# Kernel tuning notes

Hardware: AMD Instinct MI355X
Metric: run time of the kernel (lower is better)

## Reference

```python
import jax, jax.numpy as jnp
import numpy as np

N_NODES = 100000
N_EDGES = 1600000
IN_DIM = 128
HIDDEN = 128
OUT_DIM = 10
N_GRAPHS = 512
N_LAYERS = 3


def setup_inputs() -> dict:
    key = jax.random.key(0)
    ks = jax.random.split(key, 12)
    s_in = 1.0 / np.sqrt(IN_DIM)
    s_h = 1.0 / np.sqrt(HIDDEN)
    return {
        "x": jax.random.normal(ks[0], (N_NODES, IN_DIM), jnp.float32),
        "lin1_w": jax.random.normal(ks[1], (IN_DIM, HIDDEN), jnp.float32) * s_in,
        "lin1_b": jnp.zeros((HIDDEN,), jnp.float32),
        "gcn_w": jax.random.normal(ks[2], (N_LAYERS, HIDDEN, HIDDEN), jnp.float32) * s_h,
        "gcn_b": jnp.zeros((N_LAYERS, HIDDEN), jnp.float32),
        "lin_out_w": jax.random.normal(ks[3], (HIDDEN, HIDDEN), jnp.float32) * s_h,
        "lin_out_b": jnp.zeros((HIDDEN,), jnp.float32),
        "cls_w": jax.random.normal(ks[4], (HIDDEN, OUT_DIM), jnp.float32) * s_h,
        "cls_b": jnp.zeros((OUT_DIM,), jnp.float32),
        "edge_index": jax.random.randint(ks[5], (2, N_EDGES), 0, N_NODES, jnp.int64),
        "batch": jnp.sort(jax.random.randint(ks[6], (N_NODES,), 0, N_GRAPHS, jnp.int64)),
    }


def reference(x, lin1_w, lin1_b, gcn_w, gcn_b, lin_out_w, lin_out_b, cls_w, cls_b, edge_index, batch):
    n = x.shape[0]
    # GCNConv normalization with added self-loops (PyG default)
    row, col = edge_index[0], edge_index[1]
    loop = jnp.arange(n)
    row2 = jnp.concatenate([row, loop])  # source (message origin)
    col2 = jnp.concatenate([col, loop])  # target (aggregation index)
    deg = jax.ops.segment_sum(jnp.ones_like(col2, dtype=x.dtype), col2, num_segments=n)
    dinv = jax.lax.rsqrt(jnp.maximum(deg, 1.0))
    norm = (dinv[row2] * dinv[col2])[:, None]  # [E+N, 1]

    counts = jax.ops.segment_sum(jnp.ones((n,), x.dtype), batch, num_segments=N_GRAPHS)
    counts = jnp.maximum(counts, 1.0)[:, None]

    def readout_mean(h):  # global_mean_pool -> [G, H]
        return jax.ops.segment_sum(h, batch, num_segments=N_GRAPHS) / counts

    # lin1 + elu (dropout = identity in eval mode)
    h = jax.nn.elu(x @ lin1_w + lin1_b)
    reps = readout_mean(h)  # readout_layers[0]; l_sum accumulates layer reps
    for i in range(N_LAYERS):
        hw = h @ gcn_w[i]                       # [N, H]
        msg = norm * hw[row2]                   # gather + scale
        agg = jax.ops.segment_sum(msg, col2, num_segments=n)  # scatter-add
        h = jax.nn.elu(agg + gcn_b[i])          # GCNConv bias then NaOp act
        # pooling op is 'none' (remove_pooling=True): graph unchanged
        reps = reps + readout_mean(h)           # readout_layers[i+1], summed by LaOp 'l_sum'
    g = jax.nn.elu(reps @ lin_out_w + lin_out_b)
    logits = g @ cls_w + cls_b
    return jax.nn.log_softmax(logits, axis=-1)
```

## Files before the change

### kernel.cpp

```cpp
#include <hip/hip_runtime.h>
#include <hip/hip_bf16.h>
#include <math.h>

#define NN 100000
#define NE 1600000
#define HID 128
#define NG 512
#define NB 512
#define RB 196
#define PCHUNK 16384
#define NPARTB ((NE + PCHUNK - 1) / PCHUNK)
#define GEMM_GRID ((NN + 127) / 128)

typedef unsigned short ushort_t;
typedef __attribute__((ext_vector_type(8))) short bf16x8;
typedef __attribute__((ext_vector_type(8))) unsigned short ushort8_t;
typedef __attribute__((ext_vector_type(4))) float f32x4;

__device__ __forceinline__ ushort_t f2bf(float v) {
    unsigned u = __float_as_uint(v);
    unsigned r = (u + 0x7FFF + ((u >> 16) & 1)) >> 16;
    return (ushort_t)r;
}
__device__ __forceinline__ float bf2f(ushort_t u) {
    return __uint_as_float((unsigned)u << 16);
}


__global__ __launch_bounds__(256) void hist_prepw(const int* __restrict__ ecol, int* __restrict__ bcount,
                                                  const float* __restrict__ lin1_w,
                                                  const float* __restrict__ gcn_w,
                                                  ushort_t* __restrict__ wt_hi,
                                                  ushort_t* __restrict__ wt_lo) {
    if (blockIdx.x < NPARTB) {
        __shared__ int lh[NB];
        const int blk = blockIdx.x, t = threadIdx.x;
        for (int i = t; i < NB; i += 256) lh[i] = 0;
        __syncthreads();
        const int e0 = blk * PCHUNK;
        const int e1 = min(e0 + PCHUNK, NE);
        for (int e = e0 + t; e < e1; e += 256) atomicAdd(&lh[ecol[e] / RB], 1);
        __syncthreads();
        for (int i = t; i < NB; i += 256) bcount[blk * NB + i] = lh[i];
    } else {
        int mb = blockIdx.x - NPARTB;
        int m = mb >> 3;
        int chunk = mb & 7;
        const float* W = (m == 0) ? lin1_w : gcn_w + (size_t)(m - 1) * 16384;
        ushort_t* hi = wt_hi + (size_t)m * 16384;
        ushort_t* lo = wt_lo + (size_t)m * 16384;
        for (int i = chunk * 2048 + threadIdx.x; i < (chunk + 1) * 2048; i += 256) {
            int j = i & 7;
            int lane = (i >> 3) & 63;
            int ks = (i >> 9) & 3;
            int ct = (i >> 11) & 7;
            int n = ct * 16 + (lane & 15);
            int k = ks * 32 + (lane >> 4) * 8 + j;
            float v = W[k * 128 + n];
            ushort_t h = f2bf(v);
            hi[i] = h;
            lo[i] = f2bf(v - bf2f(h));
        }
    }
}

__global__ __launch_bounds__(NB) void scan_bases(const int* __restrict__ bcount, int* __restrict__ basew,
                                                 int* __restrict__ brp, int* __restrict__ rp,
                                                 const int* __restrict__ batch, float* __restrict__ invcnt) {
    __shared__ int s[NB];
    int t = threadIdx.x;
    int tot = 0;
    for (int k = 0; k < NPARTB; ++k) {
        int c = bcount[k * NB + t];
        basew[k * NB + t] = tot;
        tot += c;
    }
    s[t] = tot;
    __syncthreads();
    for (int off = 1; off < NB; off <<= 1) {
        int x = (t >= off) ? s[t - off] : 0;
        __syncthreads();
        s[t] += x;
        __syncthreads();
    }
    int ex = s[t] - tot;
    brp[t] = ex;
    if (t == NB - 1) { brp[NB] = s[t]; rp[NN] = s[t]; }

    int lo = 0, hi = NN;
    while (lo < hi) { int m = (lo + hi) >> 1; if (batch[m] < t) lo = m + 1; else hi = m; }
    int s0 = lo;
    lo = 0; hi = NN;
    while (lo < hi) { int m = (lo + hi) >> 1; if (batch[m] < t + 1) lo = m + 1; else hi = m; }
    int c = lo - s0;
    invcnt[t] = 1.0f / (float)(c > 0 ? c : 1);
}

template<bool F32A, int MODE>
__device__ __forceinline__ void gemm_body(int bid, int tid,
                                          const float* __restrict__ A,
                                          const ushort_t* __restrict__ a_bf,
                                          const ushort_t* __restrict__ wt_hi,
                                          const ushort_t* __restrict__ wt_lo,
                                          const float* __restrict__ bias,
                                          const float* __restrict__ dinv,
                                          ushort_t* __restrict__ out0,
                                          int N) {
    const int lane = tid & 63;
    const int wid = tid >> 6;
    const int rowBase = bid * 128 + wid * 32;
    const int rblk = rowBase >> 4;
    const int l15 = lane & 15, lg = lane >> 4;

    f32x4 acc[2][8];
#pragma unroll
    for (int rt = 0; rt < 2; ++rt)
#pragma unroll
        for (int ct = 0; ct < 8; ++ct) acc[rt][ct] = (f32x4){0.f, 0.f, 0.f, 0.f};

#pragma unroll
    for (int ks = 0; ks < 4; ++ks) {
        bf16x8 ahi[2], alo[2];
#pragma unroll
        for (int rt = 0; rt < 2; ++rt) {
            int r = rowBase + rt * 16 + l15;
            if (F32A) {
                float av[8];
                if (r < N) {
                    const float* ap = A + (size_t)r * 128 + ks * 32 + lg * 8;
                    float4 a0 = *(const float4*)(ap);
                    float4 a1 = *(const float4*)(ap + 4);
                    av[0] = a0.x; av[1] = a0.y; av[2] = a0.z; av[3] = a0.w;
                    av[4] = a1.x; av[5] = a1.y; av[6] = a1.z; av[7] = a1.w;
                } else {
#pragma unroll
                    for (int j = 0; j < 8; ++j) av[j] = 0.f;
                }
#pragma unroll
                for (int j = 0; j < 8; ++j) {
                    ushort_t h = f2bf(av[j]);
                    ahi[rt][j] = (short)h;
                    alo[rt][j] = (short)f2bf(av[j] - bf2f(h));
                }
            } else {
                if (r < N) {
                    ahi[rt] = *(const bf16x8*)(a_bf + (size_t)(rblk + rt) * 2048 + (ks * 4 + lg) * 128 + l15 * 8);
                } else {
                    bf16x8 z = {0, 0, 0, 0, 0, 0, 0, 0};
                    ahi[rt] = z;
                }
            }
        }
#pragma unroll
        for (int ct = 0; ct < 8; ++ct) {
            size_t boff = (size_t)(((ct * 4 + ks) * 64 + lane) * 8);
            bf16x8 bhi = *(const bf16x8*)(wt_hi + boff);
            bf16x8 blo = *(const bf16x8*)(wt_lo + boff);
            acc[0][ct] = __builtin_amdgcn_mfma_f32_16x16x32_bf16(ahi[0], bhi, acc[0][ct], 0, 0, 0);
            acc[1][ct] = __builtin_amdgcn_mfma_f32_16x16x32_bf16(ahi[1], bhi, acc[1][ct], 0, 0, 0);
            acc[0][ct] = __builtin_amdgcn_mfma_f32_16x16x32_bf16(ahi[0], blo, acc[0][ct], 0, 0, 0);
            acc[1][ct] = __builtin_amdgcn_mfma_f32_16x16x32_bf16(ahi[1], blo, acc[1][ct], 0, 0, 0);
            if (F32A) {
                acc[0][ct] = __builtin_amdgcn_mfma_f32_16x16x32_bf16(alo[0], bhi, acc[0][ct], 0, 0, 0);
                acc[1][ct] = __builtin_amdgcn_mfma_f32_16x16x32_bf16(alo[1], bhi, acc[1][ct], 0, 0, 0);
            }
        }
    }

#pragma unroll
    for (int rt = 0; rt < 2; ++rt) {
#pragma unroll
        for (int reg = 0; reg < 4; ++reg) {
            int row = rowBase + rt * 16 + lg * 4 + reg;
            if (row >= N) continue;
            if (MODE == 0) {
                int r16 = lg * 4 + reg;
#pragma unroll
                for (int ct = 0; ct < 8; ++ct) {
                    int colc = ct * 16 + l15;
                    float v = acc[rt][ct][reg] + bias[colc];
                    v = v > 0.f ? v : expf(v) - 1.f;
                    out0[(size_t)(rblk + rt) * 2048 + (colc >> 3) * 128 + r16 * 8 + (colc & 7)] = f2bf(v);
                }
            } else {
                float dv = dinv[row];
#pragma unroll
                for (int ct = 0; ct < 8; ++ct) {
                    int colc = ct * 16 + l15;
                    out0[(size_t)row * 128 + colc] = f2bf(acc[rt][ct][reg] * dv);
                }
            }
        }
    }
}

__global__ __launch_bounds__(256) void part_gemm1(const int* __restrict__ erow, const int* __restrict__ ecol,
                                                  const int* __restrict__ brp, const int* __restrict__ basew,
                                                  unsigned int* __restrict__ pairs,
                                                  const float* __restrict__ x,
                                                  const ushort_t* __restrict__ wt_hi,
                                                  const ushort_t* __restrict__ wt_lo,
                                                  const float* __restrict__ lin1_b,
                                                  ushort_t* __restrict__ h) {
    if (blockIdx.x < NPARTB) {
        __shared__ int sbase[NB];
        __shared__ int lcnt[NB];
        const int blk = blockIdx.x, t = threadIdx.x;
        for (int i = t; i < NB; i += 256) {
            sbase[i] = brp[i] + basew[blk * NB + i];
            lcnt[i] = 0;
        }
        __syncthreads();
        const int e0 = blk * PCHUNK;
        const int e1 = min(e0 + PCHUNK, NE);
        for (int e = e0 + t; e < e1; e += 256) {
            int d = ecol[e];
            int b = d / RB;
            int off = atomicAdd(&lcnt[b], 1);
            pairs[sbase[b] + off] = ((unsigned)erow[e] << 8) | (unsigned)(d - b * RB);
        }
    } else {
        gemm_body<true, 0>(blockIdx.x - NPARTB, threadIdx.x, x, nullptr, wt_hi, wt_lo,
                           lin1_b, nullptr, h, NN);
    }
}

__global__ __launch_bounds__(256) void fill_readout0(const unsigned int* __restrict__ pairs, const int* __restrict__ brp,
                                                     int* __restrict__ rp, float* __restrict__ dinv,
                                                     int* __restrict__ csrc,
                                                     const ushort_t* __restrict__ h,
                                                     const int* __restrict__ batch,
                                                     const float* __restrict__ invcnt,
                                                     float* __restrict__ reps) {
    if (blockIdx.x < NB) {
        __shared__ int cnt[RB];
        __shared__ int cur[RB];
        __shared__ int sc[256];
        const int b = blockIdx.x, t = threadIdx.x;
        const int nbase = b * RB;
        const int s = brp[b], e = brp[b + 1];
        for (int i = t; i < RB; i += 256) cnt[i] = 0;
        __syncthreads();
        for (int i = s + t; i < e; i += 256) atomicAdd(&cnt[pairs[i] & 255u], 1);
        __syncthreads();
        int v = (t < RB) ? cnt[t] : 0;
        sc[t] = v;
        __syncthreads();
        for (int off = 1; off < 256; off <<= 1) {
            int x = (t >= off) ? sc[t - off] : 0;
            __syncthreads();
            sc[t] += x;
            __syncthreads();
        }
        if (t < RB) {
            int ex = s + sc[t] - v;
            int node = nbase + t;
            if (node < NN) {
                rp[node] = ex;
                dinv[node] = rsqrtf((float)v + 1.0f);
            }
            cur[t] = ex;
        }
        __syncthreads();
        for (int i = s + t; i < e; i += 256) {
            unsigned int p = pairs[i];
            int slot = atomicAdd(&cur[p & 255u], 1);
            csrc[slot] = (int)(p >> 8);
        }
    } else {
        int bb = blockIdx.x - NB;
        int g = bb >> 2;
        int part = bb & 3;
        int lo = 0, hi = NN;
        while (lo < hi) { int m = (lo + hi) >> 1; if (batch[m] < g) lo = m + 1; else hi = m; }
        int s = lo;
        lo = 0; hi = NN;
        while (lo < hi) { int m = (lo + hi) >> 1; if (batch[m] < g + 1) lo = m + 1; else hi = m; }
        int e = lo;

        __shared__ float sh[16][136];
        int ns = (int)(threadIdx.x >> 4);
        int L  = (int)(threadIdx.x & 15);
        int c8 = L << 3;
        float acc[8] = {};
        for (int v = s + part + ns * 4; v < e; v += 64) {
            ushort8_t t = *(const ushort8_t*)(h + (size_t)(v >> 4) * 2048 + L * 128 + (v & 15) * 8);
#pragma unroll
            for (int j = 0; j < 8; ++j) acc[j] += bf2f(t[j]);
        }
#pragma unroll
        for (int j = 0; j < 8; ++j) sh[ns][c8 + j] = acc[j];
        __syncthreads();
        if (threadIdx.x < 128) {
            int c = (int)threadIdx.x;
            float sum = 0.f;
#pragma unroll
            for (int k = 0; k < 16; ++k) sum += sh[k][c];
            unsafeAtomicAdd(&reps[(size_t)g * 128 + c], sum * invcnt[g]);
        }
    }
}

__global__ __launch_bounds__(256) void gemm_gcn(const ushort_t* __restrict__ a_bf,
                                                const ushort_t* __restrict__ wt_hi,
                                                const ushort_t* __restrict__ wt_lo,
                                                const float* __restrict__ dinv,
                                                ushort_t* __restrict__ hwb) {
    gemm_body<false, 1>(blockIdx.x, threadIdx.x, nullptr, a_bf, wt_hi, wt_lo,
                        nullptr, dinv, hwb, NN);
}

__global__ __launch_bounds__(256) void gather_agg(const int* __restrict__ rp,
                                                  const int* __restrict__ csrc,
                                                  const float* __restrict__ dinv,
                                                  const ushort_t* __restrict__ hwb,
                                                  const float* __restrict__ bias,
                                                  const int* __restrict__ batch,
                                                  const float* __restrict__ invcnt,
                                                  float* __restrict__ reps,
                                                  ushort_t* __restrict__ h_out) {
    __shared__ float sh[16][136];
    __shared__ int gid[16];
    const int v0 = blockIdx.x * 16;
    const int ns = (int)(threadIdx.x >> 4);
    int v = v0 + ns;
    int L = (int)(threadIdx.x & 15);
    int c8 = L << 3;
    if (threadIdx.x < 16) {
        int bidx = v0 + (int)threadIdx.x;
        if (bidx > NN - 1) bidx = NN - 1;
        gid[threadIdx.x] = batch[bidx];
    }

    float acc[8] = {};
    if (v < NN) {
        int s = rp[v], e = rp[v + 1];
        int i = s;
        for (; i + 16 <= e; i += 16) {
            int u[16];
#pragma unroll
            for (int k = 0; k < 16; ++k) u[k] = csrc[i + k];
            ushort8_t r[16];
#pragma unroll
            for (int k = 0; k < 16; ++k) r[k] = *(const ushort8_t*)(hwb + (size_t)u[k] * 128 + c8);
#pragma unroll
            for (int k = 0; k < 16; ++k)
#pragma unroll
                for (int j = 0; j < 8; ++j) acc[j] += bf2f(r[k][j]);
        }
        for (; i + 8 <= e; i += 8) {
            int u[8];
#pragma unroll
            for (int k = 0; k < 8; ++k) u[k] = csrc[i + k];
            ushort8_t r[8];
#pragma unroll
            for (int k = 0; k < 8; ++k) r[k] = *(const ushort8_t*)(hwb + (size_t)u[k] * 128 + c8);
#pragma unroll
            for (int k = 0; k < 8; ++k)
#pragma unroll
                for (int j = 0; j < 8; ++j) acc[j] += bf2f(r[k][j]);
        }
        for (; i < e; ++i) {
            int u = csrc[i];
            ushort8_t r0 = *(const ushort8_t*)(hwb + (size_t)u * 128 + c8);
#pragma unroll
            for (int j = 0; j < 8; ++j) acc[j] += bf2f(r0[j]);
        }

        float di = dinv[v];
        ushort8_t sv = *(const ushort8_t*)(hwb + (size_t)v * 128 + c8);
        ushort8_t o;
#pragma unroll
        for (int j = 0; j < 8; ++j) {
            float t = di * (acc[j] + bf2f(sv[j])) + bias[c8 + j];
            t = t > 0.f ? t : expf(t) - 1.f;
            acc[j] = t;
            o[j] = f2bf(t);
        }
        *(ushort8_t*)(h_out + (size_t)blockIdx.x * 2048 + L * 128 + ns * 8) = o;
    } else {
#pragma unroll
        for (int j = 0; j < 8; ++j) acc[j] = 0.f;
    }

#pragma unroll
    for (int j = 0; j < 8; ++j) sh[ns][c8 + j] = acc[j];
    __syncthreads();
    if (threadIdx.x < 128) {
        int c = (int)threadIdx.x;
        int nvalid = NN - v0;
        if (nvalid > 16) nvalid = 16;
        float run = sh[0][c];
        int cg = gid[0];
        for (int k = 1; k < nvalid; ++k) {
            int g2 = gid[k];
            if (g2 != cg) {
                unsafeAtomicAdd(&reps[(size_t)cg * 128 + c], run * invcnt[cg]);
                run = 0.f;
                cg = g2;
            }
            run += sh[k][c];
        }
        unsafeAtomicAdd(&reps[(size_t)cg * 128 + c], run * invcnt[cg]);
    }
}

__global__ __launch_bounds__(128) void head_fused(const float* __restrict__ reps,
                                                  const float* __restrict__ wout,
                                                  const float* __restrict__ bout,
                                                  const float* __restrict__ cw,
                                                  const float* __restrict__ cb,
                                                  float* __restrict__ out) {
    __shared__ float rrow[128];
    __shared__ float gg[128];
    __shared__ float lg[10];
    int t = threadIdx.x;
    int g = blockIdx.x;
    rrow[t] = reps[(size_t)g * 128 + t];
    __syncthreads();
    float a = bout[t];
    for (int k = 0; k < 128; ++k) a = fmaf(rrow[k], wout[k * 128 + t], a);
    a = a > 0.f ? a : expf(a) - 1.f;
    gg[t] = a;
    __syncthreads();
    if (t < 10) {
        float s = cb[t];
        for (int k = 0; k < 128; ++k) s = fmaf(gg[k], cw[k * 10 + t], s);
        lg[t] = s;
    }
    __syncthreads();
    if (t == 0) {
        float m = lg[0];
#pragma unroll
        for (int j = 1; j < 10; ++j) m = fmaxf(m, lg[j]);
        float se = 0.f;
#pragma unroll
        for (int j = 0; j < 10; ++j) se += expf(lg[j] - m);
        float L = logf(se);
#pragma unroll
        for (int j = 0; j < 10; ++j) out[(size_t)g * 10 + j] = lg[j] - m - L;
    }
}

extern "C" void kernel_launch(void* const* d_in, const int* in_sizes, int n_in,
                              void* d_out, int out_size, void* d_ws, size_t ws_size,
                              hipStream_t stream) {
    const float* x        = (const float*)d_in[0];
    const float* lin1_w   = (const float*)d_in[1];
    const float* lin1_b   = (const float*)d_in[2];
    const float* gcn_w    = (const float*)d_in[3];
    const float* gcn_b    = (const float*)d_in[4];
    const float* lin_out_w= (const float*)d_in[5];
    const float* lin_out_b= (const float*)d_in[6];
    const float* cls_w    = (const float*)d_in[7];
    const float* cls_b    = (const float*)d_in[8];
    const int*   ei       = (const int*)d_in[9];
    const int*   batch    = (const int*)d_in[10];
    float* out = (float*)d_out;

    const int* erow = ei;
    const int* ecol = ei + NE;

    ushort_t* h     = (ushort_t*)d_ws;
    ushort_t* hwb   = h + (size_t)NN * 128;
    float*    dinv  = (float*)(hwb + (size_t)NN * 128);
    float*    reps  = dinv + NN;
    float*    invcnt= reps + (size_t)NG * 128;
    int*      rp    = (int*)(invcnt + NG);
    int*      csrc  = rp + NN + 1;
    int*      brp   = csrc + NE;
    int*      bcount= brp + NB + 1;
    int*      basew = bcount + NPARTB * NB;
    ushort_t* wt_hi = (ushort_t*)(basew + NPARTB * NB);
    ushort_t* wt_lo = wt_hi + 4 * 16384;
    unsigned int* pairs = (unsigned int*)(wt_lo + 4 * 16384);

    hipMemsetAsync(reps, 0, (size_t)NG * 128 * sizeof(float), stream);

    hist_prepw<<<NPARTB + 32, 256, 0, stream>>>(ecol, bcount, lin1_w, gcn_w, wt_hi, wt_lo);
    scan_bases<<<1, NB, 0, stream>>>(bcount, basew, brp, rp, batch, invcnt);
    part_gemm1<<<NPARTB + GEMM_GRID, 256, 0, stream>>>(erow, ecol, brp, basew, pairs,
                                                       x, wt_hi, wt_lo, lin1_b, h);
    fill_readout0<<<NB + NG * 4, 256, 0, stream>>>(pairs, brp, rp, dinv, csrc,
                                                   h, batch, invcnt, reps);

    for (int i = 0; i < 3; ++i) {
        gemm_gcn<<<GEMM_GRID, 256, 0, stream>>>(h, wt_hi + (size_t)(i + 1) * 16384,
                                                wt_lo + (size_t)(i + 1) * 16384,
                                                dinv, hwb);
        gather_agg<<<(NN + 15) / 16, 256, 0, stream>>>(rp, csrc, dinv, hwb,
                                                       gcn_b + (size_t)i * 128,
                                                       batch, invcnt, reps, h);
    }

    head_fused<<<NG, 128, 0, stream>>>(reps, lin_out_w, lin_out_b, cls_w, cls_b, out);
}
```

Measured before the change: 427.1 us.

## Split gather-aggregate across column slices with 128-node chunks per block

The neighbour-gather kernel is reorganised. Each block now covers 128 nodes for one 16-column slice, so eight consecutive blocks share the same node chunk, and two threads handle each node. The 16-wide unrolled gather loop is dropped and the per-graph readout reduction is redone per slice. The aim is better parallelism and cache locality per column slice. In exchange, each neighbour row is read as narrow 32-byte pieces by eight separate blocks, and the CSR index arrays are re-read eight times.

```diff
diff --git a/kernel.cpp b/kernel.cpp
--- a/kernel.cpp
+++ b/kernel.cpp
@@ -11,6 +11,8 @@
 #define PCHUNK 16384
 #define NPARTB ((NE + PCHUNK - 1) / PCHUNK)
 #define GEMM_GRID ((NN + 127) / 128)
+#define GCHUNK 128
+#define NCHUNKS ((NN + GCHUNK - 1) / GCHUNK)
 
 typedef unsigned short ushort_t;
 typedef __attribute__((ext_vector_type(8))) short bf16x8;
@@ -319,35 +321,27 @@
                                                   const float* __restrict__ invcnt,
                                                   float* __restrict__ reps,
                                                   ushort_t* __restrict__ h_out) {
-    __shared__ float sh[16][136];
-    __shared__ int gid[16];
-    const int v0 = blockIdx.x * 16;
-    const int ns = (int)(threadIdx.x >> 4);
+    const int cs = (int)(blockIdx.x & 7);
+    const int chunk = (int)(blockIdx.x >> 3);
+    const int v0 = chunk * GCHUNK;
+    const int t = (int)threadIdx.x;
+    const int ns = t >> 1;
+    const int half = t & 1;
+    const int c8 = cs * 16 + half * 8;
     int v = v0 + ns;
-    int L = (int)(threadIdx.x & 15);
-    int c8 = L << 3;
-    if (threadIdx.x < 16) {
-        int bidx = v0 + (int)threadIdx.x;
+
+    __shared__ float sh[128][16];
+    __shared__ int gid[128];
+    if (t < 128) {
+        int bidx = v0 + t;
         if (bidx > NN - 1) bidx = NN - 1;
-        gid[threadIdx.x] = batch[bidx];
+        gid[t] = batch[bidx];
     }
 
     float acc[8] = {};
     if (v < NN) {
         int s = rp[v], e = rp[v + 1];
         int i = s;
-        for (; i + 16 <= e; i += 16) {
-            int u[16];
-#pragma unroll
-            for (int k = 0; k < 16; ++k) u[k] = csrc[i + k];
-            ushort8_t r[16];
-#pragma unroll
-            for (int k = 0; k < 16; ++k) r[k] = *(const ushort8_t*)(hwb + (size_t)u[k] * 128 + c8);
-#pragma unroll
-            for (int k = 0; k < 16; ++k)
-#pragma unroll
-                for (int j = 0; j < 8; ++j) acc[j] += bf2f(r[k][j]);
-        }
         for (; i + 8 <= e; i += 8) {
             int u[8];
 #pragma unroll
@@ -372,36 +366,37 @@
         ushort8_t o;
 #pragma unroll
         for (int j = 0; j < 8; ++j) {
-            float t = di * (acc[j] + bf2f(sv[j])) + bias[c8 + j];
-            t = t > 0.f ? t : expf(t) - 1.f;
-            acc[j] = t;
-            o[j] = f2bf(t);
-        }
-        *(ushort8_t*)(h_out + (size_t)blockIdx.x * 2048 + L * 128 + ns * 8) = o;
+            float tv = di * (acc[j] + bf2f(sv[j])) + bias[c8 + j];
+            tv = tv > 0.f ? tv : expf(tv) - 1.f;
+            acc[j] = tv;
+            o[j] = f2bf(tv);
+        }
+        *(ushort8_t*)(h_out + (size_t)(v >> 4) * 2048 + (c8 >> 3) * 128 + (v & 15) * 8) = o;
     } else {
 #pragma unroll
         for (int j = 0; j < 8; ++j) acc[j] = 0.f;
     }
 
 #pragma unroll
-    for (int j = 0; j < 8; ++j) sh[ns][c8 + j] = acc[j];
+    for (int j = 0; j < 8; ++j) sh[ns][half * 8 + j] = acc[j];
     __syncthreads();
-    if (threadIdx.x < 128) {
-        int c = (int)threadIdx.x;
-        int nvalid = NN - v0;
-        if (nvalid > 16) nvalid = 16;
-        float run = sh[0][c];
-        int cg = gid[0];
-        for (int k = 1; k < nvalid; ++k) {
-            int g2 = gid[k];
+    if (t < 128) {
+        int sc = t >> 4;
+        int c  = t & 15;
+        int base = sc * 16;
+        float run = sh[base][c];
+        int cg = gid[base];
+#pragma unroll
+        for (int k = 1; k < 16; ++k) {
+            int g2 = gid[base + k];
             if (g2 != cg) {
-                unsafeAtomicAdd(&reps[(size_t)cg * 128 + c], run * invcnt[cg]);
+                unsafeAtomicAdd(&reps[(size_t)cg * 128 + cs * 16 + c], run * invcnt[cg]);
                 run = 0.f;
                 cg = g2;
             }
-            run += sh[k][c];
-        }
-        unsafeAtomicAdd(&reps[(size_t)cg * 128 + c], run * invcnt[cg]);
+            run += sh[base + k][c];
+        }
+        unsafeAtomicAdd(&reps[(size_t)cg * 128 + cs * 16 + c], run * invcnt[cg]);
     }
 }
 
@@ -488,9 +483,9 @@
         gemm_gcn<<<GEMM_GRID, 256, 0, stream>>>(h, wt_hi + (size_t)(i + 1) * 16384,
                                                 wt_lo + (size_t)(i + 1) * 16384,
                                                 dinv, hwb);
-        gather_agg<<<(NN + 15) / 16, 256, 0, stream>>>(rp, csrc, dinv, hwb,
-                                                       gcn_b + (size_t)i * 128,
-                                                       batch, invcnt, reps, h);
+        gather_agg<<<NCHUNKS * 8, 256, 0, stream>>>(rp, csrc, dinv, hwb,
+                                                    gcn_b + (size_t)i * 128,
+                                                    batch, invcnt, reps, h);
     }
 
     head_fused<<<NG, 128, 0, stream>>>(reps, lin_out_w, lin_out_b, cls_w, cls_b, out);
```

Result: slower. 826.1 us (+93.4%).
